# Performance work log

Measured on AMD Instinct MI355X. Metric: run time of the kernel, lower is better.

Reference implementation:

```python
import itertools
import jax, jax.numpy as jnp
import numpy as np

EPS = 1e-15
B, K, H, W = 64, 8, 128, 128


def setup_inputs() -> dict:
    key = jax.random.key(0)
    k1, k2 = jax.random.split(key)
    pred_masks = jax.random.uniform(k1, (B, K, H, W), dtype=jnp.float32)
    aug_masks = jax.random.uniform(k2, (B, K, H, W), dtype=jnp.float32)
    return {"pred_masks": pred_masks, "aug_masks": aug_masks}


def _mask_kl_div(pred, true):
    # true * (log(true+eps) - log(pred+eps)), mean over (H, W)
    return (true * (jnp.log(true + EPS) - jnp.log(pred + EPS))).mean(axis=(-2, -1))


# all K! permutations, precomputed once (K=8 -> 40320 perms)
_PERMS = jnp.asarray(np.array(list(itertools.permutations(range(K))), dtype=np.int32))


def reference(pred_masks, aug_masks):
    b, k, h, w = pred_masks.shape
    t = aug_masks  # targets are detached in torch for the cost matrix
    # Fused pairwise KL cost matrix (avoids the (B,K,K,H,W) broadcast):
    # C[b,i,j] = mean_hw[ t_j*log(t_j+eps) ] - mean_hw[ t_j*log(p_i+eps) ]
    ent = (t * jnp.log(t + EPS)).mean(axis=(-2, -1))          # (B, K) over j
    cross = jnp.einsum('bjhw,bihw->bij', t, jnp.log(pred_masks + EPS)) / (h * w)
    C = ent[:, None, :] - cross                                # (B, K, K)
    # exact linear assignment via exhaustive search over K! permutations
    rows = jnp.arange(k)
    costs = C[:, rows[None, :], _PERMS].sum(axis=-1)           # (B, K!)
    R2C = _PERMS[jnp.argmin(costs, axis=1)]                    # (B, K) col for each row
    # permute rows: out[b, i] = pred[b, argsort(R2C)[b, i]]
    row_perm = jnp.argsort(R2C, axis=1)
    pred_perm = jnp.take_along_axis(pred_masks, row_perm[:, :, None, None], axis=1)
    l = _mask_kl_div(pred_perm, t)                             # (B, K)
    return l.mean(), pred_perm[..., None]
```

## Files before the change

kernel.cpp:

```cpp
#include <hip/hip_runtime.h>


#define BB 64
#define KK 8
#define HW 16384
#define CH 16
#define CHUNK 1024
#define EPSF 1e-15f

struct MaskTab {
    unsigned char masks[255];
    int off[9];
};

constexpr MaskTab make_tab() {
    MaskTab t{};
    int idx = 0;
    for (int p = 1; p <= 8; ++p) {
        t.off[p - 1] = idx;
        for (int m = 1; m < 256; ++m) {
            int c = 0;
            for (int b = 0; b < 8; ++b) c += (m >> b) & 1;
            if (c == p) t.masks[idx++] = (unsigned char)m;
        }
    }
    t.off[8] = idx;
    return t;
}

__constant__ MaskTab kTab = make_tab();

__device__ __forceinline__ float dot4(float4 t, float4 l) {
    return t.x * l.x + t.y * l.y + t.z * l.z + t.w * l.w;
}

__global__ __launch_bounds__(256) void cost_kernel(const float* __restrict__ pred,
                                                   const float* __restrict__ aug,
                                                   float* __restrict__ part)
{
    const int blk   = blockIdx.x;
    const int b     = blk >> 4;
    const int chunk = blk & 15;
    const int tid   = threadIdx.x;
    const int wave  = tid >> 6;
    const int lane  = tid & 63;

    const float* p0  = pred + (size_t)b * (KK * HW) + (size_t)(2 * wave) * HW + chunk * CHUNK;
    const float* p1  = p0 + HW;
    const float* tb  = aug + (size_t)b * (KK * HW) + chunk * CHUNK;
    const float* t0b = tb + (size_t)(2 * wave) * HW;
    const float* t1b = t0b + HW;

    float acc[16];
#pragma unroll
    for (int v = 0; v < 16; ++v) acc[v] = 0.f;
    float e0 = 0.f, e1 = 0.f;

#pragma unroll
    for (int it = 0; it < 4; ++it) {
        const int off = it * 256 + lane * 4;

        float4 a4 = *(const float4*)(p0 + off);
        float4 c4 = *(const float4*)(p1 + off);
        float4 la, lc;
        la.x = __logf(a4.x + EPSF); la.y = __logf(a4.y + EPSF);
        la.z = __logf(a4.z + EPSF); la.w = __logf(a4.w + EPSF);
        lc.x = __logf(c4.x + EPSF); lc.y = __logf(c4.y + EPSF);
        lc.z = __logf(c4.z + EPSF); lc.w = __logf(c4.w + EPSF);

#pragma unroll
        for (int j = 0; j < 8; ++j) {
            float4 t4 = *(const float4*)(tb + (size_t)j * HW + off);
            acc[j]     += dot4(t4, la);
            acc[8 + j] += dot4(t4, lc);
        }

        float4 t0 = *(const float4*)(t0b + off);
        float4 t1 = *(const float4*)(t1b + off);
        e0 += t0.x * __logf(t0.x + EPSF) + t0.y * __logf(t0.y + EPSF)
            + t0.z * __logf(t0.z + EPSF) + t0.w * __logf(t0.w + EPSF);
        e1 += t1.x * __logf(t1.x + EPSF) + t1.y * __logf(t1.y + EPSF)
            + t1.z * __logf(t1.z + EPSF) + t1.w * __logf(t1.w + EPSF);
    }

#pragma unroll
    for (int v = 0; v < 16; ++v) {
        float s = acc[v];
#pragma unroll
        for (int d = 1; d < 64; d <<= 1) s += __shfl_xor(s, d);
        acc[v] = s;
    }
#pragma unroll
    for (int d = 1; d < 64; d <<= 1) e0 += __shfl_xor(e0, d);
#pragma unroll
    for (int d = 1; d < 64; d <<= 1) e1 += __shfl_xor(e1, d);

    if (lane == 0) {
        float* dst = part + (size_t)blk * 72;
#pragma unroll
        for (int j = 0; j < 8; ++j) {
            dst[16 * wave + j]     = acc[j];
            dst[16 * wave + 8 + j] = acc[8 + j];
        }
        dst[64 + 2 * wave]     = e0;
        dst[64 + 2 * wave + 1] = e1;
    }
}

__global__ __launch_bounds__(64) void assign_kernel(const float* __restrict__ part,
                                                    int* __restrict__ ws_inv,
                                                    float* __restrict__ ws_loss)
{
    __shared__ float C[64];
    __shared__ float dp[256];
    __shared__ int   choice[256];

    const int b    = blockIdx.x;
    const int lane = threadIdx.x;
    const float* pb = part + (size_t)b * CH * 72;

    float s = 0.f;
#pragma unroll
    for (int c = 0; c < CH; ++c) s += pb[c * 72 + lane];
    float e = 0.f;
    if (lane < 8) {
#pragma unroll
        for (int c = 0; c < CH; ++c) e += pb[c * 72 + 64 + lane];
    }
    const float entj = __shfl(e, lane & 7);
    C[lane] = entj - s;
    if (lane == 0) dp[0] = 0.f;
    __syncthreads();

    const int grp = lane >> 3;
    const int j   = lane & 7;

    for (int p = 1; p <= 8; ++p) {
        const int start = kTab.off[p - 1];
        const int end   = kTab.off[p];
        const float* Crow = &C[(p - 1) * 8];
        for (int base = start; base < end; base += 8) {
            const int mi = base + grp;
            if (mi < end) {
                const int M = kTab.masks[mi];
                float v  = 1e30f;
                int   bj = 0;
                if (M & (1 << j)) {
                    v  = dp[M ^ (1 << j)] + Crow[j];
                    bj = j;
                }
#pragma unroll
                for (int d = 1; d < 8; d <<= 1) {
                    float ov = __shfl_xor(v, d);
                    int   oj = __shfl_xor(bj, d);
                    if (ov < v) { v = ov; bj = oj; }
                }
                if (j == 0) { dp[M] = v; choice[M] = bj; }
            }
        }
        __syncthreads();
    }

    if (lane == 0) {
        int mask = 255;
        for (int r = 7; r >= 0; --r) {
            const int jj = choice[mask];
            ws_inv[b * 8 + jj] = r;
            mask ^= 1 << jj;
        }
        ws_loss[b] = dp[255] * (1.0f / (16384.0f * 512.0f));
    }
}

__global__ __launch_bounds__(256) void permute_kernel(const float* __restrict__ pred,
                                                      const int* __restrict__ ws_inv,
                                                      const float* __restrict__ ws_loss,
                                                      float* __restrict__ out)
{
    const int blk    = blockIdx.x;
    const int pair   = blk >> 3;
    const int cchunk = blk & 7;
    const int b      = pair >> 3;

    const int src_row = ws_inv[pair];

    const float* src = pred + ((size_t)b * 8 + src_row) * HW + cchunk * 2048;
    float*       dst = out + 1 + (size_t)pair * HW + cchunk * 2048;

    const int t = threadIdx.x;
#pragma unroll
    for (int m = 0; m < 8; ++m) dst[t + m * 256] = src[t + m * 256];

    if (blk == 0 && t < 64) {
        float v = ws_loss[t];
#pragma unroll
        for (int d = 1; d < 64; d <<= 1) v += __shfl_xor(v, d);
        if (t == 0) out[0] = v;
    }
}

extern "C" void kernel_launch(void* const* d_in, const int* in_sizes, int n_in,
                              void* d_out, int out_size, void* d_ws, size_t ws_size,
                              hipStream_t stream) {
    const float* pred = (const float*)d_in[0];
    const float* aug  = (const float*)d_in[1];
    float* out = (float*)d_out;

    float* part    = (float*)d_ws;
    int*   ws_inv  = (int*)(part + BB * CH * 72);
    float* ws_loss = (float*)(ws_inv + BB * KK);

    cost_kernel<<<dim3(BB * CH), dim3(256), 0, stream>>>(pred, aug, part);
    assign_kernel<<<dim3(BB), dim3(64), 0, stream>>>(part, ws_inv, ws_loss);
    permute_kernel<<<dim3(512 * 8), dim3(256), 0, stream>>>(pred, ws_inv, ws_loss, out);
}
```

Measured before the change: 125.7 us.

## Fuse assignment DP into permute kernel and reuse target loads for entropy

Merges the assignment kernel into the permute kernel. Each of 1024 blocks redundantly recomputes the per-batch cost matrix and the subset DP with 256 threads (32 masks per step), then copies half of one permuted row using float4 stores aligned to the out+1 offset. The loss is accumulated with one atomicAdd per batch into an output zeroed by a memset. The cost kernel now computes the entropy from the target float4 it already loaded, dropping two redundant loads per iteration. This removes one kernel launch and the workspace round-trip, but the DP work is now repeated 16 times per batch and the load side of the copy is scalar.

```diff
diff --git a/kernel.cpp b/kernel.cpp
--- a/kernel.cpp
+++ b/kernel.cpp
@@ -32,6 +32,13 @@
 
 __device__ __forceinline__ float dot4(float4 t, float4 l) {
     return t.x * l.x + t.y * l.y + t.z * l.z + t.w * l.w;
+}
+
+__device__ __forceinline__ float4 log4(float4 a) {
+    float4 r;
+    r.x = __logf(a.x + EPSF); r.y = __logf(a.y + EPSF);
+    r.z = __logf(a.z + EPSF); r.w = __logf(a.w + EPSF);
+    return r;
 }
 
 __global__ __launch_bounds__(256) void cost_kernel(const float* __restrict__ pred,
@@ -44,12 +51,11 @@
     const int tid   = threadIdx.x;
     const int wave  = tid >> 6;
     const int lane  = tid & 63;
-
-    const float* p0  = pred + (size_t)b * (KK * HW) + (size_t)(2 * wave) * HW + chunk * CHUNK;
-    const float* p1  = p0 + HW;
-    const float* tb  = aug + (size_t)b * (KK * HW) + chunk * CHUNK;
-    const float* t0b = tb + (size_t)(2 * wave) * HW;
-    const float* t1b = t0b + HW;
+    const int w2    = 2 * wave;
+
+    const float* p0 = pred + (size_t)b * (KK * HW) + (size_t)w2 * HW + chunk * CHUNK;
+    const float* p1 = p0 + HW;
+    const float* tb = aug + (size_t)b * (KK * HW) + chunk * CHUNK;
 
     float acc[16];
 #pragma unroll
@@ -60,27 +66,20 @@
     for (int it = 0; it < 4; ++it) {
         const int off = it * 256 + lane * 4;
 
-        float4 a4 = *(const float4*)(p0 + off);
-        float4 c4 = *(const float4*)(p1 + off);
-        float4 la, lc;
-        la.x = __logf(a4.x + EPSF); la.y = __logf(a4.y + EPSF);
-        la.z = __logf(a4.z + EPSF); la.w = __logf(a4.w + EPSF);
-        lc.x = __logf(c4.x + EPSF); lc.y = __logf(c4.y + EPSF);
-        lc.z = __logf(c4.z + EPSF); lc.w = __logf(c4.w + EPSF);
+        float4 la = log4(*(const float4*)(p0 + off));
+        float4 lc = log4(*(const float4*)(p1 + off));
 
 #pragma unroll
         for (int j = 0; j < 8; ++j) {
             float4 t4 = *(const float4*)(tb + (size_t)j * HW + off);
             acc[j]     += dot4(t4, la);
             acc[8 + j] += dot4(t4, lc);
-        }
-
-        float4 t0 = *(const float4*)(t0b + off);
-        float4 t1 = *(const float4*)(t1b + off);
-        e0 += t0.x * __logf(t0.x + EPSF) + t0.y * __logf(t0.y + EPSF)
-            + t0.z * __logf(t0.z + EPSF) + t0.w * __logf(t0.w + EPSF);
-        e1 += t1.x * __logf(t1.x + EPSF) + t1.y * __logf(t1.y + EPSF)
-            + t1.z * __logf(t1.z + EPSF) + t1.w * __logf(t1.w + EPSF);
+            if (j == w2) {
+                e0 += dot4(t4, log4(t4));
+            } else if (j == w2 + 1) {
+                e1 += dot4(t4, log4(t4));
+            }
+        }
     }
 
 #pragma unroll
@@ -102,44 +101,47 @@
             dst[16 * wave + j]     = acc[j];
             dst[16 * wave + 8 + j] = acc[8 + j];
         }
-        dst[64 + 2 * wave]     = e0;
-        dst[64 + 2 * wave + 1] = e1;
-    }
-}
-
-__global__ __launch_bounds__(64) void assign_kernel(const float* __restrict__ part,
-                                                    int* __restrict__ ws_inv,
-                                                    float* __restrict__ ws_loss)
+        dst[64 + w2]     = e0;
+        dst[64 + w2 + 1] = e1;
+    }
+}
+
+__global__ __launch_bounds__(256) void permute_kernel(const float* __restrict__ pred,
+                                                      const float* __restrict__ part,
+                                                      float* __restrict__ out)
 {
+    __shared__ float red[72];
     __shared__ float C[64];
     __shared__ float dp[256];
     __shared__ int   choice[256];
-
-    const int b    = blockIdx.x;
-    const int lane = threadIdx.x;
+    __shared__ int   inv8[8];
+
+    const int g    = blockIdx.x;
+    const int p    = g >> 1;
+    const int half = g & 1;
+    const int b    = p >> 3;
+    const int tid  = threadIdx.x;
+
     const float* pb = part + (size_t)b * CH * 72;
-
-    float s = 0.f;
-#pragma unroll
-    for (int c = 0; c < CH; ++c) s += pb[c * 72 + lane];
-    float e = 0.f;
-    if (lane < 8) {
-#pragma unroll
-        for (int c = 0; c < CH; ++c) e += pb[c * 72 + 64 + lane];
-    }
-    const float entj = __shfl(e, lane & 7);
-    C[lane] = entj - s;
-    if (lane == 0) dp[0] = 0.f;
+    if (tid < 72) {
+        float s = 0.f;
+#pragma unroll
+        for (int c = 0; c < CH; ++c) s += pb[c * 72 + tid];
+        red[tid] = s;
+    }
     __syncthreads();
-
-    const int grp = lane >> 3;
-    const int j   = lane & 7;
-
-    for (int p = 1; p <= 8; ++p) {
-        const int start = kTab.off[p - 1];
-        const int end   = kTab.off[p];
-        const float* Crow = &C[(p - 1) * 8];
-        for (int base = start; base < end; base += 8) {
+    if (tid < 64) C[tid] = red[64 + (tid & 7)] - red[tid];
+    if (tid == 0) dp[0] = 0.f;
+    __syncthreads();
+
+    const int grp = tid >> 3;
+    const int j   = tid & 7;
+
+    for (int lvl = 1; lvl <= 8; ++lvl) {
+        const int start = kTab.off[lvl - 1];
+        const int end   = kTab.off[lvl];
+        const float* Crow = &C[(lvl - 1) * 8];
+        for (int base = start; base < end; base += 32) {
             const int mi = base + grp;
             if (mi < end) {
                 const int M = kTab.masks[mi];
@@ -161,41 +163,34 @@
         __syncthreads();
     }
 
-    if (lane == 0) {
+    if (tid == 0) {
         int mask = 255;
         for (int r = 7; r >= 0; --r) {
             const int jj = choice[mask];
-            ws_inv[b * 8 + jj] = r;
+            inv8[jj] = r;
             mask ^= 1 << jj;
         }
-        ws_loss[b] = dp[255] * (1.0f / (16384.0f * 512.0f));
-    }
-}
-
-__global__ __launch_bounds__(256) void permute_kernel(const float* __restrict__ pred,
-                                                      const int* __restrict__ ws_inv,
-                                                      const float* __restrict__ ws_loss,
-                                                      float* __restrict__ out)
-{
-    const int blk    = blockIdx.x;
-    const int pair   = blk >> 3;
-    const int cchunk = blk & 7;
-    const int b      = pair >> 3;
-
-    const int src_row = ws_inv[pair];
-
-    const float* src = pred + ((size_t)b * 8 + src_row) * HW + cchunk * 2048;
-    float*       dst = out + 1 + (size_t)pair * HW + cchunk * 2048;
-
-    const int t = threadIdx.x;
-#pragma unroll
-    for (int m = 0; m < 8; ++m) dst[t + m * 256] = src[t + m * 256];
-
-    if (blk == 0 && t < 64) {
-        float v = ws_loss[t];
-#pragma unroll
-        for (int d = 1; d < 64; d <<= 1) v += __shfl_xor(v, d);
-        if (t == 0) out[0] = v;
+        if (g == (b << 4))
+            atomicAdd(out, dp[255] * (1.0f / (16384.0f * 512.0f)));
+    }
+    __syncthreads();
+
+    const int src_row = inv8[p & 7];
+    const float* src = pred + ((size_t)(b << 3) + src_row) * HW;
+    float*       drow = out + 1 + (size_t)p * HW;
+
+#pragma unroll
+    for (int m = 0; m < 8; ++m) {
+        const int f = half * 2048 + tid + 256 * m;
+        const int e = 3 + 4 * f;
+        if (f < 4095) {
+            float4 v;
+            v.x = src[e]; v.y = src[e + 1]; v.z = src[e + 2]; v.w = src[e + 3];
+            *(float4*)(drow + e) = v;
+        } else {
+            drow[0] = src[0]; drow[1] = src[1]; drow[2] = src[2];
+            drow[16383] = src[16383];
+        }
     }
 }
 
@@ -205,12 +200,10 @@
     const float* pred = (const float*)d_in[0];
     const float* aug  = (const float*)d_in[1];
     float* out = (float*)d_out;
-
-    float* part    = (float*)d_ws;
-    int*   ws_inv  = (int*)(part + BB * CH * 72);
-    float* ws_loss = (float*)(ws_inv + BB * KK);
+    float* part = (float*)d_ws;
+
+    hipMemsetAsync(d_out, 0, sizeof(float), stream);
 
     cost_kernel<<<dim3(BB * CH), dim3(256), 0, stream>>>(pred, aug, part);
-    assign_kernel<<<dim3(BB), dim3(64), 0, stream>>>(part, ws_inv, ws_loss);
-    permute_kernel<<<dim3(512 * 8), dim3(256), 0, stream>>>(pred, ws_inv, ws_loss, out);
-}
+    permute_kernel<<<dim3(1024), dim3(256), 0, stream>>>(pred, part, out);
+}
```

New measurement: 123.3 us. About the same (-1.9%).
